# Kernel optimization log

Hardware: AMD Instinct MI355X
Metric: run time of the kernel (lower is better)

Reference implementation:

```python
import jax, jax.numpy as jnp
import numpy as np

D_MODEL = 1024
N_HEADS = 16
HEAD_DIM = D_MODEL // N_HEADS


def rotate_half(x):
    # interleaved rotate: (-x_odd, x_even) re-interleaved
    x1 = x[..., ::2]
    x2 = x[..., 1::2]
    return jnp.stack((-x2, x1), axis=-1).reshape(x.shape)


def rope_tables(seq_len, dim, dtype):
    inv_freq = 1.0 / (10000.0 ** (jnp.arange(0, dim, 2, dtype=jnp.float32) / dim))
    t = jnp.arange(seq_len, dtype=jnp.float32)
    freqs = jnp.einsum('i,j->ij', t, inv_freq)          # [T, dim/2]
    emb = jnp.concatenate((freqs, freqs), axis=-1)       # [T, dim]
    return jnp.cos(emb).astype(dtype)[None, None], jnp.sin(emb).astype(dtype)[None, None]


def setup_inputs() -> dict:
    key = jax.random.key(0)
    k1, k2, k3 = jax.random.split(key, 3)
    B, T, C = 2, 2048, D_MODEL
    scale_in = 1.0 / np.sqrt(C)
    return {
        'x': jax.random.normal(k1, (B, T, C), dtype=jnp.float32),
        'attention_mask': jnp.ones((B, T), dtype=jnp.int32),
        'qkv_w': jax.random.normal(k2, (3 * C, C), dtype=jnp.float32) * scale_in,
        'qkv_b': jnp.zeros((3 * C,), dtype=jnp.float32),
        'out_w': jax.random.normal(k3, (C, C), dtype=jnp.float32) * scale_in,
        'out_b': jnp.zeros((C,), dtype=jnp.float32),
    }


def reference(x, attention_mask, qkv_w, qkv_b, out_w, out_b):
    B, T, C = x.shape
    H, Dh = N_HEADS, HEAD_DIM
    qkv = x @ qkv_w.T + qkv_b                             # [B,T,3C]
    q, k, v = jnp.split(qkv, 3, axis=-1)
    q = q.reshape(B, T, H, Dh).transpose(0, 2, 1, 3)      # [B,H,T,Dh]
    k = k.reshape(B, T, H, Dh).transpose(0, 2, 1, 3)
    v = v.reshape(B, T, H, Dh).transpose(0, 2, 1, 3)
    cos, sin = rope_tables(T, Dh, x.dtype)                # [1,1,T,Dh]
    q = q * cos + rotate_half(q) * sin
    k = k * cos + rotate_half(k) * sin
    att = jnp.einsum('bhqd,bhkd->bhqk', q, k) / jnp.sqrt(jnp.array(Dh, x.dtype))
    causal = jnp.tril(jnp.ones((T, T), dtype=bool))[None, None]
    key_mask = attention_mask.astype(bool)[:, None, None, :]
    neg_inf = jnp.array(-jnp.inf, att.dtype)
    att = jnp.where(causal & key_mask, att, neg_inf)
    att = jax.nn.softmax(att, axis=-1)
    query_mask = attention_mask.astype(bool)[:, None, :, None]
    att = att * query_mask
    y = jnp.einsum('bhqk,bhkd->bhqd', att, v)             # [B,H,T,Dh]
    y = y.transpose(0, 2, 1, 3).reshape(B, T, C)
    y = y * attention_mask[:, :, None].astype(y.dtype)
    y = y @ out_w.T + out_b
    return y
```

## Files before the change

kernel.cpp:

```cpp
#include <hip/hip_runtime.h>
#include <hip/hip_bf16.h>

typedef __bf16 bf16;
typedef __bf16 bf16x4 __attribute__((ext_vector_type(4)));
typedef __bf16 bf16x8 __attribute__((ext_vector_type(8)));
typedef float f32x4 __attribute__((ext_vector_type(4)));
typedef unsigned int u32x4 __attribute__((ext_vector_type(4)));

#define T_LEN 2048
#define NHEAD 16
#define DHEAD 64
#define CDIM 1024
#define NB 2

__device__ __forceinline__ void g2l16(const void* g, void* l) {
    __builtin_amdgcn_global_load_lds(
        (const __attribute__((address_space(1))) unsigned int*)g,
        (__attribute__((address_space(3))) unsigned int*)l, 16, 0, 0);
}

__device__ __forceinline__ float fexp2(float x) {
    float r;
    asm("v_exp_f32 %0, %1" : "=v"(r) : "v"(x));
    return r;
}

__device__ __forceinline__ void stage_swz512(const bf16* __restrict__ g, size_t gstride,
                                             bf16* lds, int t) {
    int off = t * 16;
    int row = off >> 7;
    int lcol = (off & 127) ^ ((row & 7) << 4);
    g2l16(g + (size_t)row * gstride + (lcol >> 1), (char*)lds + off);
}

__device__ __forceinline__ bf16x8 rd_swz(const bf16* lds, int row, int colB) {
    return *(const bf16x8*)((const char*)lds + row * 128 + (colB ^ ((row & 7) << 4)));
}

__global__ __launch_bounds__(256) void prep_kernel(
    const float* __restrict__ x, const float* __restrict__ qkv_w,
    const float* __restrict__ out_w, const int* __restrict__ am,
    bf16* __restrict__ xb, bf16* __restrict__ wqb, bf16* __restrict__ wob,
    float* __restrict__ ct, float* __restrict__ st, float* __restrict__ mf,
    int* __restrict__ mflag) {
    int bid = blockIdx.x;
    if (bid < 4096) {
        int i = bid * 256 + threadIdx.x;
        const float* src; bf16* dst; int j;
        if (i < 524288)      { src = x;     dst = xb;  j = i; }
        else if (i < 917504) { src = qkv_w; dst = wqb; j = i - 524288; }
        else                 { src = out_w; dst = wob; j = i - 917504; }
        const float4* p = (const float4*)src + (size_t)j * 2;
        float4 a = p[0], b = p[1];
        bf16x8 o;
        o[0] = (bf16)a.x; o[1] = (bf16)a.y; o[2] = (bf16)a.z; o[3] = (bf16)a.w;
        o[4] = (bf16)b.x; o[5] = (bf16)b.y; o[6] = (bf16)b.z; o[7] = (bf16)b.w;
        ((bf16x8*)dst)[j] = o;
    } else if (bid < 4608) {
        int i = (bid - 4096) * 256 + threadIdx.x;
        int t = i >> 6, d = i & 63;
        float ex = (float)(2 * (d & 31)) / 64.0f;
        float inv = powf(10000.0f, -ex);
        float ang = (float)t * inv;
        ct[i] = cosf(ang);
        st[i] = sinf(ang);
    } else {
        int i = (bid - 4608) * 256 + threadIdx.x;
        int v = am[i];
        mf[i] = (v != 0) ? 0.0f : -1e30f;
        unsigned long long bz = __ballot(v == 0);
        if ((threadIdx.x & 63) == 0) mflag[i >> 6] = (bz != 0) ? 1 : 0;
    }
}

__global__ __launch_bounds__(512, 6) void gemm_qkv_kernel(
    const bf16* __restrict__ xb, const bf16* __restrict__ wb,
    const float* __restrict__ bias,
    const float* __restrict__ ct, const float* __restrict__ st,
    bf16* __restrict__ qg, bf16* __restrict__ kg, bf16* __restrict__ vt) {
    __shared__ __align__(16) bf16 smem[2 * 128 * 64];
    bf16* sA = smem;
    bf16* sB = smem + 128 * 64;
    int m0 = blockIdx.x * 128, n0 = blockIdx.y * 128;
    int t = threadIdx.x, w = t >> 6, l = t & 63;
    int wm = w & 3, wn = w >> 2;
    int l15 = l & 15, lhi = l >> 4;
    f32x4 acc[2][4] = {};
    for (int k0 = 0; k0 < CDIM; k0 += 64) {
#pragma unroll
        for (int c = 0; c < 2; c++) {
            int off = c * 8192 + t * 16;
            int row = off >> 7;
            int lcol = (off & 127) ^ ((row & 7) << 4);
            g2l16(xb + (size_t)(m0 + row) * CDIM + k0 + (lcol >> 1), (char*)sA + off);
            g2l16(wb + (size_t)(n0 + row) * CDIM + k0 + (lcol >> 1), (char*)sB + off);
        }
        __syncthreads();
#pragma unroll
        for (int ks = 0; ks < 2; ks++) {
            bf16x8 af[2], bfr[4];
#pragma unroll
            for (int mt = 0; mt < 2; mt++)
                af[mt] = rd_swz(sA, wm * 32 + mt * 16 + l15, ks * 64 + lhi * 16);
#pragma unroll
            for (int nt = 0; nt < 4; nt++)
                bfr[nt] = rd_swz(sB, wn * 64 + nt * 16 + l15, ks * 64 + lhi * 16);
#pragma unroll
            for (int mt = 0; mt < 2; mt++)
#pragma unroll
                for (int nt = 0; nt < 4; nt++)
                    acc[mt][nt] = __builtin_amdgcn_mfma_f32_16x16x32_bf16(
                        af[mt], bfr[nt], acc[mt][nt], 0, 0, 0);
        }
        __syncthreads();
    }
    int bb = m0 >> 11, tt0 = m0 & 2047;
    if (n0 >= 2048) {
        bf16* sT = smem;
#pragma unroll
        for (int pass = 0; pass < 2; pass++) {
            __syncthreads();
            if (wn == pass) {
#pragma unroll
                for (int nt = 0; nt < 4; nt++) {
                    int dl = nt * 16 + l15;
                    float cb = bias[n0 + pass * 64 + dl];
#pragma unroll
                    for (int mt = 0; mt < 2; mt++) {
                        bf16x4 pv;
#pragma unroll
                        for (int r = 0; r < 4; r++) pv[r] = (bf16)(acc[mt][nt][r] + cb);
                        *(bf16x4*)(sT + dl * 136 + wm * 32 + mt * 16 + lhi * 4) = pv;
                    }
                }
            }
            __syncthreads();
            int h_p = ((n0 & 1023) >> 6) + pass;
            size_t vbase = ((size_t)(bb * NHEAD + h_p)) * T_LEN * DHEAD + tt0;
#pragma unroll
            for (int c = 0; c < 2; c++) {
                int cid = c * 512 + t;
                int d = cid >> 4, ch = cid & 15;
                *(bf16x8*)(vt + vbase + (size_t)d * T_LEN + ch * 8) =
                    *(const bf16x8*)(sT + d * 136 + ch * 8);
            }
        }
        return;
    }
    int sec = n0 >> 10;
    bf16* og = (sec == 0) ? qg : kg;
    float oscale = (sec == 0) ? 0.125f * 1.44269504f : 1.0f;
#pragma unroll
    for (int nt = 0; nt < 4; nt++) {
        int col = n0 + wn * 64 + nt * 16 + l15;
        int cc = col & 1023;
        int h = cc >> 6, d = cc & 63;
        float cb = bias[col];
        size_t hb = ((size_t)(bb * NHEAD + h)) * T_LEN * DHEAD;
#pragma unroll
        for (int mt = 0; mt < 2; mt++) {
#pragma unroll
            for (int r = 0; r < 4; r++) {
                int tt = tt0 + wm * 32 + mt * 16 + lhi * 4 + r;
                float v = acc[mt][nt][r] + cb;
                float p = __shfl_xor(v, 1);
                float cs = ct[tt * 64 + d], sn = st[tt * 64 + d];
                float o = (d & 1) ? (v * cs + p * sn) : (v * cs - p * sn);
                og[hb + (size_t)tt * DHEAD + d] = (bf16)(o * oscale);
            }
        }
    }
}

__global__ __launch_bounds__(512, 4) void attn_kernel(
    const bf16* __restrict__ qg, const bf16* __restrict__ kg, const bf16* __restrict__ vt,
    const float* __restrict__ maskf, const int* __restrict__ mflag,
    bf16* __restrict__ yb) {
    __shared__ __align__(16) bf16 sK[2][64 * 64];
    __shared__ __align__(16) bf16 sV[2][64 * 64];
    int lin = blockIdx.x;
    int xcd = lin & 7, idx = lin >> 3;
    int group = idx >> 4, pos = idx & 15;
    int qt0 = (pos & 1) ? (pos >> 1) : (15 - (pos >> 1));
    int qt = (group & 2) ? (15 - qt0) : qt0;
    int pair = xcd * 4 + group;
    int h = pair & 15, b = pair >> 4;
    int q0 = qt * 128;
    int t = threadIdx.x, w = t >> 6, l = t & 63;
    int l15 = l & 15, lhi = l >> 4;
    const size_t head_off = ((size_t)(b * NHEAD + h)) * T_LEN * DHEAD;
    const bf16* qb = qg + head_off;
    const bf16* kb = kg + head_off;
    const bf16* vb = vt + head_off;
    const float* mrow = maskf + b * T_LEN;
    const int* mfl = mflag + b * (T_LEN / 64);
    const int wq0 = q0 + w * 16;
    const int qrow_l = wq0 + l15;
    bf16x8 qf[2];
    {
        qf[0] = *(const bf16x8*)(qb + (size_t)qrow_l * DHEAD + lhi * 8);
        qf[1] = *(const bf16x8*)(qb + (size_t)qrow_l * DHEAD + 32 + lhi * 8);
    }
    const u32x4 onesu = {0x3F803F80u, 0x3F803F80u, 0x3F803F80u, 0x3F803F80u};
    const bf16x8 ones8 = __builtin_bit_cast(bf16x8, onesu);
    float m_ = -1e30f;
    f32x4 lsv = {};
    f32x4 accy[4] = {};
    stage_swz512(kb, DHEAD, sK[0], t);
    stage_swz512(vb, T_LEN, sV[0], t);
    __syncthreads();
    int cur = 0;
    const int kv_end = q0 + 64;
    for (int kv0 = 0; kv0 <= kv_end; kv0 += 64) {
        if (kv0 + 64 <= kv_end) {
            stage_swz512(kb + (size_t)(kv0 + 64) * DHEAD, DHEAD, sK[cur ^ 1], t);
            stage_swz512(vb + (kv0 + 64), T_LEN, sV[cur ^ 1], t);
        }
        if (kv0 <= wq0 + 15) {
            f32x4 s[4] = {};
            __builtin_amdgcn_s_setprio(1);
#pragma unroll
            for (int c = 0; c < 4; c++)
#pragma unroll
                for (int ks = 0; ks < 2; ks++) {
                    bf16x8 kf = rd_swz(sK[cur], c * 16 + l15, ks * 64 + lhi * 16);
                    s[c] = __builtin_amdgcn_mfma_f32_16x16x32_bf16(kf, qf[ks], s[c], 0, 0, 0);
                }
            __builtin_amdgcn_s_setprio(0);
            bool diag = (kv0 + 63 > wq0);
            int needmask = mfl[kv0 >> 6];
            float mxl = -1e30f;
            if (!needmask && !diag) {
#pragma unroll
                for (int c = 0; c < 4; c++)
#pragma unroll
                    for (int r = 0; r < 4; r++) mxl = fmaxf(mxl, s[c][r]);
            } else {
#pragma unroll
                for (int c = 0; c < 4; c++) {
                    float mpv[4] = {0.f, 0.f, 0.f, 0.f};
                    if (needmask) {
                        float4 mq = *(const float4*)(mrow + kv0 + c * 16 + lhi * 4);
                        mpv[0] = mq.x; mpv[1] = mq.y; mpv[2] = mq.z; mpv[3] = mq.w;
                    }
#pragma unroll
                    for (int r = 0; r < 4; r++) {
                        float sv = s[c][r] + mpv[r];
                        if (diag && (kv0 + c * 16 + lhi * 4 + r > qrow_l)) sv = -1e30f;
                        s[c][r] = sv;
                        mxl = fmaxf(mxl, sv);
                    }
                }
            }
            float mx = fmaxf(mxl, __shfl_xor(mxl, 16));
            mx = fmaxf(mx, __shfl_xor(mx, 32));
            if (kv0 == 0) m_ = mx;
#pragma unroll
            for (int c = 0; c < 4; c++)
#pragma unroll
                for (int r = 0; r < 4; r++) s[c][r] = fexp2(s[c][r] - m_);
            if (kv0 != 0 && !__all(mx <= m_ + 8.f)) {
                float mn = fmaxf(m_, mx);
                float scf = fexp2(m_ - mn);
                m_ = mn;
#pragma unroll
                for (int c = 0; c < 4; c++)
#pragma unroll
                    for (int r = 0; r < 4; r++) s[c][r] *= scf;
#pragma unroll
                for (int r = 0; r < 4; r++) {
                    float sr = __shfl(scf, (l & 48) + lhi * 4 + r);
                    lsv[r] *= sr;
#pragma unroll
                    for (int dt = 0; dt < 4; dt++) accy[dt][r] *= sr;
                }
            }
            __builtin_amdgcn_s_setprio(1);
#pragma unroll
            for (int g2 = 0; g2 < 2; g2++) {
                unsigned a0, a1, b0, b1;
                asm("v_cvt_pk_bf16_f32 %0, %1, %2" : "=v"(a0) : "v"(s[2 * g2][0]), "v"(s[2 * g2][1]));
                asm("v_cvt_pk_bf16_f32 %0, %1, %2" : "=v"(a1) : "v"(s[2 * g2][2]), "v"(s[2 * g2][3]));
                asm("v_cvt_pk_bf16_f32 %0, %1, %2" : "=v"(b0) : "v"(s[2 * g2 + 1][0]), "v"(s[2 * g2 + 1][1]));
                asm("v_cvt_pk_bf16_f32 %0, %1, %2" : "=v"(b1) : "v"(s[2 * g2 + 1][2]), "v"(s[2 * g2 + 1][3]));
                asm("v_permlane32_swap_b32 %0, %1" : "+v"(a0), "+v"(b0));
                asm("v_permlane16_swap_b32 %0, %1" : "+v"(a0), "+v"(b0));
                asm("v_permlane32_swap_b32 %0, %1" : "+v"(a1), "+v"(b1));
                asm("v_permlane16_swap_b32 %0, %1" : "+v"(a1), "+v"(b1));
                u32x4 pu;
                pu[0] = a0; pu[1] = a1; pu[2] = b0; pu[3] = b1;
                bf16x8 pv = __builtin_bit_cast(bf16x8, pu);
                lsv = __builtin_amdgcn_mfma_f32_16x16x32_bf16(pv, ones8, lsv, 0, 0, 0);
#pragma unroll
                for (int dt = 0; dt < 4; dt++) {
                    bf16x8 vf = rd_swz(sV[cur], dt * 16 + l15, g2 * 64 + lhi * 16);
                    accy[dt] = __builtin_amdgcn_mfma_f32_16x16x32_bf16(pv, vf, accy[dt], 0, 0, 0);
                }
            }
            __builtin_amdgcn_s_setprio(0);
        }
        __syncthreads();
        cur ^= 1;
    }
#pragma unroll
    for (int r = 0; r < 4; r++) {
        float inv = lsv[r] > 0.f ? 1.0f / lsv[r] : 0.0f;
        int rowt = wq0 + lhi * 4 + r;
        size_t obase = ((size_t)(b * T_LEN + rowt)) * CDIM + (size_t)h * DHEAD;
#pragma unroll
        for (int dt = 0; dt < 4; dt++)
            yb[obase + dt * 16 + l15] = (bf16)(accy[dt][r] * inv);
    }
}

__global__ __launch_bounds__(256) void gemm_out_kernel(
    const bf16* __restrict__ yb, const bf16* __restrict__ wb,
    const float* __restrict__ bias, float* __restrict__ out) {
    __shared__ __align__(16) bf16 sA[128 * 64];
    __shared__ __align__(16) bf16 sB[64 * 64];
    int m0 = blockIdx.x * 128, n0 = blockIdx.y * 64;
    int t = threadIdx.x, w = t >> 6, l = t & 63;
    int wm = w >> 1, wn = w & 1;
    int l15 = l & 15, lhi = l >> 4;
    f32x4 acc[4][2] = {};
    for (int k0 = 0; k0 < CDIM; k0 += 64) {
#pragma unroll
        for (int i = 0; i < 4; i++) {
            int off = i * 4096 + t * 16;
            int row = off >> 7;
            int lcol = (off & 127) ^ ((row & 7) << 4);
            g2l16(yb + (size_t)(m0 + row) * CDIM + k0 + (lcol >> 1), (char*)sA + off);
            if (i < 2)
                g2l16(wb + (size_t)(n0 + row) * CDIM + k0 + (lcol >> 1), (char*)sB + off);
        }
        __syncthreads();
#pragma unroll
        for (int ks = 0; ks < 2; ks++) {
            bf16x8 af[4], bfr[2];
#pragma unroll
            for (int mt = 0; mt < 4; mt++)
                af[mt] = rd_swz(sA, wm * 64 + mt * 16 + l15, ks * 64 + lhi * 16);
#pragma unroll
            for (int nt = 0; nt < 2; nt++)
                bfr[nt] = rd_swz(sB, wn * 32 + nt * 16 + l15, ks * 64 + lhi * 16);
#pragma unroll
            for (int mt = 0; mt < 4; mt++)
#pragma unroll
                for (int nt = 0; nt < 2; nt++)
                    acc[mt][nt] = __builtin_amdgcn_mfma_f32_16x16x32_bf16(
                        af[mt], bfr[nt], acc[mt][nt], 0, 0, 0);
        }
        __syncthreads();
    }
#pragma unroll
    for (int nt = 0; nt < 2; nt++) {
        int col = n0 + wn * 32 + nt * 16 + l15;
        float cb = bias[col];
#pragma unroll
        for (int mt = 0; mt < 4; mt++) {
#pragma unroll
            for (int r = 0; r < 4; r++) {
                int rowm = m0 + wm * 64 + mt * 16 + lhi * 4 + r;
                out[(size_t)rowm * CDIM + col] = acc[mt][nt][r] + cb;
            }
        }
    }
}

extern "C" void kernel_launch(void* const* d_in, const int* in_sizes, int n_in,
                              void* d_out, int out_size, void* d_ws, size_t ws_size,
                              hipStream_t stream) {
    const float* x      = (const float*)d_in[0];
    const int*   amask  = (const int*)d_in[1];
    const float* qkv_w  = (const float*)d_in[2];
    const float* qkv_b  = (const float*)d_in[3];
    const float* out_w  = (const float*)d_in[4];
    const float* out_b  = (const float*)d_in[5];
    float* out = (float*)d_out;

    char* ws = (char*)d_ws;
    bf16* xb  = (bf16*)(ws);
    bf16* wqb = (bf16*)(ws + (8ull  << 20));
    bf16* wob = (bf16*)(ws + (14ull << 20));
    bf16* qg  = (bf16*)(ws + (16ull << 20));
    bf16* kg  = (bf16*)(ws + (24ull << 20));
    bf16* vt  = (bf16*)(ws + (32ull << 20));
    bf16* yb  = (bf16*)(ws + (40ull << 20));
    float* ctab = (float*)(ws + (48ull << 20));
    float* stab = (float*)(ws + (48ull << 20) + (1ull << 19));
    float* mkf  = (float*)(ws + (49ull << 20));
    int*   mfg  = (int*)(ws + (49ull << 20) + (16ull << 10));

    prep_kernel<<<4624, 256, 0, stream>>>(x, qkv_w, out_w, amask,
                                          xb, wqb, wob, ctab, stab, mkf, mfg);
    gemm_qkv_kernel<<<dim3(32, 24), 512, 0, stream>>>(xb, wqb, qkv_b, ctab, stab, qg, kg, vt);
    attn_kernel<<<dim3(512), 512, 0, stream>>>(qg, kg, vt, mkf, mfg, yb);
    gemm_out_kernel<<<dim3(32, 16), 256, 0, stream>>>(yb, wob, out_b, out);
}
```

Before: 110.4 us.

## Double-buffer LDS tiles in QKV and output projection GEMMs

Both GEMM kernels now use two LDS buffers. The global-to-LDS loads for the next K tile are issued before the MFMA work on the current tile, so memory latency overlaps with compute instead of stalling at a barrier each iteration. The cost is twice the shared memory per block, which cuts how many blocks fit on a CU; the QKV kernel's launch-bounds occupancy hint drops from 6 to 4 to match.

Measured after the change: 106.2 us. 3.8% less time.

```diff
diff --git a/kernel.cpp b/kernel.cpp
--- a/kernel.cpp
+++ b/kernel.cpp
@@ -73,29 +73,42 @@
     }
 }
 
-__global__ __launch_bounds__(512, 6) void gemm_qkv_kernel(
+__global__ __launch_bounds__(512, 4) void gemm_qkv_kernel(
     const bf16* __restrict__ xb, const bf16* __restrict__ wb,
     const float* __restrict__ bias,
     const float* __restrict__ ct, const float* __restrict__ st,
     bf16* __restrict__ qg, bf16* __restrict__ kg, bf16* __restrict__ vt) {
-    __shared__ __align__(16) bf16 smem[2 * 128 * 64];
-    bf16* sA = smem;
-    bf16* sB = smem + 128 * 64;
+    __shared__ __align__(16) bf16 smem[2][2 * 128 * 64];
     int m0 = blockIdx.x * 128, n0 = blockIdx.y * 128;
     int t = threadIdx.x, w = t >> 6, l = t & 63;
     int wm = w & 3, wn = w >> 2;
     int l15 = l & 15, lhi = l >> 4;
     f32x4 acc[2][4] = {};
+#pragma unroll
+    for (int c = 0; c < 2; c++) {
+        int off = c * 8192 + t * 16;
+        int row = off >> 7;
+        int lcol = (off & 127) ^ ((row & 7) << 4);
+        g2l16(xb + (size_t)(m0 + row) * CDIM + (lcol >> 1), (char*)smem[0] + off);
+        g2l16(wb + (size_t)(n0 + row) * CDIM + (lcol >> 1), (char*)(smem[0] + 128 * 64) + off);
+    }
+    __syncthreads();
+    int cur = 0;
     for (int k0 = 0; k0 < CDIM; k0 += 64) {
-#pragma unroll
-        for (int c = 0; c < 2; c++) {
-            int off = c * 8192 + t * 16;
-            int row = off >> 7;
-            int lcol = (off & 127) ^ ((row & 7) << 4);
-            g2l16(xb + (size_t)(m0 + row) * CDIM + k0 + (lcol >> 1), (char*)sA + off);
-            g2l16(wb + (size_t)(n0 + row) * CDIM + k0 + (lcol >> 1), (char*)sB + off);
-        }
-        __syncthreads();
+        if (k0 + 64 < CDIM) {
+#pragma unroll
+            for (int c = 0; c < 2; c++) {
+                int off = c * 8192 + t * 16;
+                int row = off >> 7;
+                int lcol = (off & 127) ^ ((row & 7) << 4);
+                g2l16(xb + (size_t)(m0 + row) * CDIM + k0 + 64 + (lcol >> 1),
+                      (char*)smem[cur ^ 1] + off);
+                g2l16(wb + (size_t)(n0 + row) * CDIM + k0 + 64 + (lcol >> 1),
+                      (char*)(smem[cur ^ 1] + 128 * 64) + off);
+            }
+        }
+        bf16* sA = smem[cur];
+        bf16* sB = smem[cur] + 128 * 64;
 #pragma unroll
         for (int ks = 0; ks < 2; ks++) {
             bf16x8 af[2], bfr[4];
@@ -113,10 +126,11 @@
                         af[mt], bfr[nt], acc[mt][nt], 0, 0, 0);
         }
         __syncthreads();
+        cur ^= 1;
     }
     int bb = m0 >> 11, tt0 = m0 & 2047;
     if (n0 >= 2048) {
-        bf16* sT = smem;
+        bf16* sT = (bf16*)smem;
 #pragma unroll
         for (int pass = 0; pass < 2; pass++) {
             __syncthreads();
@@ -316,24 +330,40 @@
 __global__ __launch_bounds__(256) void gemm_out_kernel(
     const bf16* __restrict__ yb, const bf16* __restrict__ wb,
     const float* __restrict__ bias, float* __restrict__ out) {
-    __shared__ __align__(16) bf16 sA[128 * 64];
-    __shared__ __align__(16) bf16 sB[64 * 64];
+    __shared__ __align__(16) bf16 smem[2][128 * 64 + 64 * 64];
     int m0 = blockIdx.x * 128, n0 = blockIdx.y * 64;
     int t = threadIdx.x, w = t >> 6, l = t & 63;
     int wm = w >> 1, wn = w & 1;
     int l15 = l & 15, lhi = l >> 4;
     f32x4 acc[4][2] = {};
+#pragma unroll
+    for (int i = 0; i < 4; i++) {
+        int off = i * 4096 + t * 16;
+        int row = off >> 7;
+        int lcol = (off & 127) ^ ((row & 7) << 4);
+        g2l16(yb + (size_t)(m0 + row) * CDIM + (lcol >> 1), (char*)smem[0] + off);
+        if (i < 2)
+            g2l16(wb + (size_t)(n0 + row) * CDIM + (lcol >> 1),
+                  (char*)(smem[0] + 128 * 64) + off);
+    }
+    __syncthreads();
+    int cur = 0;
     for (int k0 = 0; k0 < CDIM; k0 += 64) {
-#pragma unroll
-        for (int i = 0; i < 4; i++) {
-            int off = i * 4096 + t * 16;
-            int row = off >> 7;
-            int lcol = (off & 127) ^ ((row & 7) << 4);
-            g2l16(yb + (size_t)(m0 + row) * CDIM + k0 + (lcol >> 1), (char*)sA + off);
-            if (i < 2)
-                g2l16(wb + (size_t)(n0 + row) * CDIM + k0 + (lcol >> 1), (char*)sB + off);
-        }
-        __syncthreads();
+        if (k0 + 64 < CDIM) {
+#pragma unroll
+            for (int i = 0; i < 4; i++) {
+                int off = i * 4096 + t * 16;
+                int row = off >> 7;
+                int lcol = (off & 127) ^ ((row & 7) << 4);
+                g2l16(yb + (size_t)(m0 + row) * CDIM + k0 + 64 + (lcol >> 1),
+                      (char*)smem[cur ^ 1] + off);
+                if (i < 2)
+                    g2l16(wb + (size_t)(n0 + row) * CDIM + k0 + 64 + (lcol >> 1),
+                          (char*)(smem[cur ^ 1] + 128 * 64) + off);
+            }
+        }
+        bf16* sA = smem[cur];
+        bf16* sB = smem[cur] + 128 * 64;
 #pragma unroll
         for (int ks = 0; ks < 2; ks++) {
             bf16x8 af[4], bfr[2];
@@ -351,6 +381,7 @@
                         af[mt], bfr[nt], acc[mt][nt], 0, 0, 0);
         }
         __syncthreads();
+        cur ^= 1;
     }
 #pragma unroll
     for (int nt = 0; nt < 2; nt++) {
```
